# Kernel optimization log

Hardware: AMD Instinct MI355X
Metric: run time of the kernel (lower is better)

## Reference

```python
import jax, jax.numpy as jnp
import numpy as np
from jax import lax

B, N, M, K = 8, 8192, 2000, 16       # batch, raw pts, subsampled pts, neighbors
C1, C2, OUT = 128, 256, 100          # backbone widths, output_embed_size


def _fps(coords, m):
    """Farthest point sampling. coords [B,N,3] -> indices [B,m] (int32)."""
    b, n, _ = coords.shape
    init_last = jnp.zeros((b,), jnp.int32)

    def body(carry, _):
        mind, last = carry
        p = jnp.take_along_axis(coords, last[:, None, None], axis=1)  # [b,1,3]
        d = jnp.sum((coords - p) ** 2, axis=-1)                        # [b,n]
        mind = jnp.minimum(mind, d)
        nxt = jnp.argmax(mind, axis=-1).astype(jnp.int32)
        return (mind, nxt), nxt

    init = (jnp.full((b, n), 1e30, coords.dtype), init_last)
    _, rest = lax.scan(body, init, None, length=m - 1)                 # [m-1,b]
    return jnp.concatenate([init_last[None], rest], axis=0).T          # [b,m]


def _gather(src, idx):
    # src [B,N,C], idx [B,...] -> [B,...,C]
    return jax.vmap(lambda s, i: s[i])(src, idx)


def _knn(q, src, k):
    # squared-distance via |q|^2+|s|^2-2q.s to avoid a [B,M,N,3] intermediate
    d2 = (jnp.sum(q * q, -1)[:, :, None]
          + jnp.sum(src * src, -1)[:, None, :]
          - 2.0 * jnp.einsum('bmd,bnd->bmn', q, src))
    return lax.top_k(-d2, k)[1]                                        # [B,M,k]


def setup_inputs() -> dict:
    key = jax.random.key(0)
    ks = jax.random.split(key, 3)
    x = jax.random.uniform(ks[0], (B, N, 3), jnp.float32)
    W1 = jax.random.normal(ks[1], (6, C1), jnp.float32) * 0.1
    b1 = jnp.zeros((C1,), jnp.float32)
    W2 = jax.random.normal(ks[2], (3 + C1, C2), jnp.float32) * 0.1
    b2 = jnp.zeros((C2,), jnp.float32)
    return {"x": x, "W1": W1, "b1": b1, "W2": W2, "b2": b2}


def reference(x, W1, b1, W2, b2):
    coords = x
    cg = lax.stop_gradient(coords)          # indices are non-differentiable
    fps_idx = _fps(cg, M)                   # [B,M]
    sub = _gather(coords, fps_idx)          # [B,M,3]
    sub_g = lax.stop_gradient(sub)

    # --- point-conv layer 1: neighbors among raw points, feats = coords ---
    idx1 = _knn(sub_g, cg, K)               # [B,M,K]
    ngh = _gather(coords, idx1)             # [B,M,K,3]
    rel1 = ngh - sub[:, :, None, :]
    h1 = jax.nn.relu(jnp.einsum('bmkf,fc->bmkc',
                                jnp.concatenate([rel1, ngh], -1), W1) + b1)
    f1 = jnp.max(h1, axis=2)                # [B,M,C1]

    # --- point-conv layer 2: neighbors among subsampled points ---
    idx2 = _knn(sub_g, sub_g, K)            # [B,M,K]
    ngh2 = _gather(sub, idx2)               # [B,M,K,3]
    rel2 = ngh2 - sub[:, :, None, :]
    fg = _gather(f1, idx2)                  # [B,M,K,C1]
    h2 = jax.nn.relu(jnp.einsum('bmkf,fc->bmkc',
                                jnp.concatenate([rel2, fg], -1), W2) + b2)
    f2 = jnp.max(h2, axis=2)                # [B,M,C2]

    # --- fused adaptive max+avg pool: M % OUT == 0 -> uniform windows ---
    feat = jnp.transpose(f2, (0, 2, 1))     # [B,C2,M]
    windows = feat.reshape(B, C2, OUT, M // OUT)
    return jnp.max(windows, axis=-1) + jnp.mean(windows, axis=-1)  # [B,C2,OUT]
```

## Files before the change

### kernel.cpp

```cpp
#include <hip/hip_runtime.h>

#define B_    8
#define N_    8192
#define M_    2000
#define K_    16
#define C1_   128
#define C2_   256
#define OUT_  100
#define SUBP_ 2048

__global__ __launch_bounds__(256) void prep_kernel(const float* __restrict__ x,
                                                   float4* __restrict__ coords4,
                                                   float4* __restrict__ sub4) {
    int i = blockIdx.x * 256 + threadIdx.x;
    if (i < B_ * N_) {
        float xx = x[i*3+0], yy = x[i*3+1], zz = x[i*3+2];
        float ss = fmaf(zz, zz, fmaf(yy, yy, xx*xx));
        coords4[i] = make_float4(xx, yy, zz, ss);
    }
    if (i < B_ * (SUBP_ - M_)) {
        int b = i / (SUBP_ - M_), j = i % (SUBP_ - M_);
        sub4[b*SUBP_ + M_ + j] = make_float4(1e15f, 1e15f, 1e15f, 3e30f);
    }
}

#define FPS_T 512
#define FPS_P 16

__device__ __forceinline__ unsigned long long umax64(unsigned long long a, unsigned long long b) {
    return a > b ? a : b;
}

template<int CTRL>
__device__ __forceinline__ unsigned long long dpp_max_u64(unsigned long long v) {
    int lo = __builtin_amdgcn_update_dpp(0, (int)(unsigned)(v & 0xFFFFFFFFull), CTRL, 0xF, 0xF, true);
    int hi = __builtin_amdgcn_update_dpp(0, (int)(v >> 32),                     CTRL, 0xF, 0xF, true);
    unsigned long long o = ((unsigned long long)(unsigned)hi << 32) | (unsigned)lo;
    return umax64(v, o);
}

__device__ __forceinline__ int spread3(int v) {
    return (v & 1) | ((v & 2) << 2) | ((v & 4) << 4);
}

__global__ __launch_bounds__(FPS_T, 1) void fps_kernel(const float4* __restrict__ coords4,
                                                       float4* __restrict__ sub4) {
    int b = blockIdx.x;
    int t = threadIdx.x;
    int w = t >> 6, lane = t & 63;
    const float4* C = coords4 + b * N_;

    __shared__ float4 Clds[N_];
    __shared__ unsigned short sidx[N_];
    __shared__ unsigned int hist[512];
    __shared__ __align__(16) unsigned long long wkey[2][8];

    if (t < 512) hist[t] = 0u;
    __syncthreads();

    int cellv[FPS_P];
#pragma unroll
    for (int j = 0; j < FPS_P; ++j) {
        int i = t + j*FPS_T;
        float4 p = C[i];
        Clds[i] = p;
        int cx = (int)(p.x * 8.0f); cx = cx < 0 ? 0 : (cx > 7 ? 7 : cx);
        int cy = (int)(p.y * 8.0f); cy = cy < 0 ? 0 : (cy > 7 ? 7 : cy);
        int cz = (int)(p.z * 8.0f); cz = cz < 0 ? 0 : (cz > 7 ? 7 : cz);
        int cell = (spread3(cx) << 2) | (spread3(cy) << 1) | spread3(cz);
        cellv[j] = cell;
        atomicAdd(&hist[cell], 1u);
    }
    __syncthreads();

    if (w == 0) {
        unsigned loc[8], tot = 0u;
#pragma unroll
        for (int c2 = 0; c2 < 8; ++c2) { loc[c2] = hist[lane*8 + c2]; tot += loc[c2]; }
        unsigned pre = tot;
#pragma unroll
        for (int d = 1; d < 64; d <<= 1) {
            unsigned o = __shfl_up(pre, d, 64);
            if (lane >= (unsigned)d) pre += o;
        }
        unsigned run = pre - tot;
#pragma unroll
        for (int c2 = 0; c2 < 8; ++c2) { unsigned v = loc[c2]; hist[lane*8 + c2] = run; run += v; }
    }
    __syncthreads();

#pragma unroll
    for (int j = 0; j < FPS_P; ++j) {
        int i = t + j*FPS_T;
        unsigned pos = atomicAdd(&hist[cellv[j]], 1u);
        sidx[pos] = (unsigned short)i;
    }
    __syncthreads();

    float px_[FPS_P], py_[FPS_P], pz_[FPS_P], mind[FPS_P];
    unsigned inv_[FPS_P];
    float bx0 =  1e30f, by0 =  1e30f, bz0 =  1e30f;
    float bx1 = -1e30f, by1 = -1e30f, bz1 = -1e30f;
#pragma unroll
    for (int j = 0; j < FPS_P; ++j) {
        int o = (int)sidx[t*FPS_P + j];
        float4 p = Clds[o];
        px_[j] = p.x; py_[j] = p.y; pz_[j] = p.z;
        mind[j] = 1e30f;
        inv_[j] = 0xFFFFFFFFu - (unsigned)o;
        bx0 = fminf(bx0, p.x); bx1 = fmaxf(bx1, p.x);
        by0 = fminf(by0, p.y); by1 = fmaxf(by1, p.y);
        bz0 = fminf(bz0, p.z); bz1 = fmaxf(bz1, p.z);
    }

    float4 P0 = Clds[0];
    if (t == 0) sub4[b*SUBP_] = P0;
    float Px = P0.x, Py = P0.y, Pz = P0.z;
    unsigned long long ckey = ((unsigned long long)__float_as_uint(1e30f) << 32);

    for (int i = 1; i < M_; ++i) {
        float qx = fminf(fmaxf(Px, bx0), bx1);
        float qy = fminf(fmaxf(Py, by0), by1);
        float qz = fminf(fmaxf(Pz, bz0), bz1);
        float ddx = Px - qx, ddy = Py - qy, ddz = Pz - qz;
        float dminsq = fmaf(ddz, ddz, fmaf(ddy, ddy, ddx*ddx));
        float maxm = __uint_as_float((unsigned)(ckey >> 32));
        if (dminsq * 0.999999f < maxm) {
            float runmax = -3.4e38f;
#pragma unroll
            for (int j = 0; j < FPS_P; ++j) {
                float dx = px_[j] - Px, dy = py_[j] - Py, dz = pz_[j] - Pz;
                float d = fmaf(dz, dz, fmaf(dy, dy, dx*dx));
                float m = fminf(mind[j], d);
                mind[j] = m;
                runmax = fmaxf(runmax, m);
            }
            unsigned ib = 0u;
#pragma unroll
            for (int j = 0; j < FPS_P; ++j) {
                unsigned cand = inv_[j] > ib ? inv_[j] : ib;
                ib = (mind[j] == runmax) ? cand : ib;
            }
            ckey = ((unsigned long long)__float_as_uint(runmax) << 32) | (unsigned long long)ib;
        }
        unsigned long long best = ckey;
        best = dpp_max_u64<0x111>(best);
        best = dpp_max_u64<0x112>(best);
        best = dpp_max_u64<0x114>(best);
        best = dpp_max_u64<0x118>(best);
        best = dpp_max_u64<0x142>(best);
        best = dpp_max_u64<0x143>(best);
        if (lane == 63) wkey[i & 1][w] = best;
        __syncthreads();
        const ulonglong2* wk2 = (const ulonglong2*)wkey[i & 1];
        ulonglong2 q0 = wk2[0], q1 = wk2[1], q2 = wk2[2], q3 = wk2[3];
        unsigned long long gk = umax64(umax64(umax64(q0.x, q0.y), umax64(q1.x, q1.y)),
                                       umax64(umax64(q2.x, q2.y), umax64(q3.x, q3.y)));
        int last = (int)(0xFFFFFFFFu - (unsigned)(gk & 0xFFFFFFFFull));
        float4 P4 = Clds[last];
        Px = P4.x; Py = P4.y; Pz = P4.z;
        if (t == 0) sub4[b*SUBP_ + i] = P4;
    }
}

template<int NCH, int PITCH>
__global__ __launch_bounds__(256) void knn_kernel(const float4* __restrict__ cand,
                                                  const float4* __restrict__ qarr,
                                                  int* __restrict__ outIdx) {
    int lane = threadIdx.x & 63;
    int q = blockIdx.x * 4 + (threadIdx.x >> 6);
    int b = q / M_, m = q % M_;
    const float4* Cb = cand + b * PITCH;
    float4 Q = qarr[b * SUBP_ + m];

    float v[16];
#pragma unroll
    for (int tt = 0; tt < 16; ++tt) v[tt] = 3.4e38f;

#pragma unroll 2
    for (int j = 0; j < NCH; ++j) {
        float4 c = Cb[j*64 + lane];
        float dot = fmaf(c.z, Q.z, fmaf(c.y, Q.y, c.x * Q.x));
        float d = fmaf(-2.0f, dot, Q.w + c.w);
        v[15] = fminf(v[15], d);
#pragma unroll
        for (int tt = 15; tt >= 1; --tt) {
            float lo = fminf(v[tt-1], v[tt]);
            float hi = fmaxf(v[tt-1], v[tt]);
            v[tt-1] = lo; v[tt] = hi;
        }
    }

    float T = 0.0f;
    for (int r = 0; r < 16; ++r) {
        float g = v[0];
#pragma unroll
        for (int s = 1; s < 64; s <<= 1) g = fminf(g, __shfl_xor(g, s, 64));
        unsigned long long mk = __ballot(v[0] == g);
        int fl = __ffsll(mk) - 1;
        if (lane == fl) {
#pragma unroll
            for (int tt = 0; tt < 15; ++tt) v[tt] = v[tt+1];
            v[15] = 3.4e38f;
        }
        T = g;
    }

    unsigned long long mlt = (1ull << lane) - 1ull;
    int base = q * K_;
    int cnt = 0;
    for (int j = 0; j < NCH; ++j) {
        float4 c = Cb[j*64 + lane];
        float dot = fmaf(c.z, Q.z, fmaf(c.y, Q.y, c.x * Q.x));
        float d = fmaf(-2.0f, dot, Q.w + c.w);
        bool lt = d < T;
        unsigned long long m1 = __ballot(lt);
        if (lt) outIdx[base + cnt + __popcll(m1 & mlt)] = j*64 + lane;
        cnt += __popcll(m1);
    }
    int rem = K_ - cnt;
    for (int j = 0; j < NCH && rem > 0; ++j) {
        float4 c = Cb[j*64 + lane];
        float dot = fmaf(c.z, Q.z, fmaf(c.y, Q.y, c.x * Q.x));
        float d = fmaf(-2.0f, dot, Q.w + c.w);
        bool eq = (d == T);
        unsigned long long m2 = __ballot(eq);
        int bef = __popcll(m2 & mlt);
        if (eq && bef < rem) outIdx[base + cnt + bef] = j*64 + lane;
        int take = __popcll(m2); if (take > rem) take = rem;
        cnt += take; rem -= take;
    }
}

__global__ __launch_bounds__(128) void layer1_kernel(const float4* __restrict__ coords4,
        const float4* __restrict__ sub4, const int* __restrict__ idx1,
        const float* __restrict__ W1, const float* __restrict__ b1,
        float* __restrict__ f1) {
    int q = blockIdx.x;
    int b = q / M_, m = q % M_;
    int c = threadIdx.x;
    __shared__ float4 ngh[K_];
    if (c < K_) ngh[c] = coords4[b*N_ + idx1[q*K_ + c]];
    __syncthreads();
    float4 Q = sub4[b*SUBP_ + m];
    float w0 = W1[c],        w1 = W1[C1_ + c],   w2 = W1[2*C1_ + c];
    float w3 = W1[3*C1_ + c], w4 = W1[4*C1_ + c], w5 = W1[5*C1_ + c];
    float bias = b1[c];
    float mx = -3.4e38f;
#pragma unroll
    for (int k = 0; k < K_; ++k) {
        float4 n = ngh[k];
        float rx = n.x - Q.x, ry = n.y - Q.y, rz = n.z - Q.z;
        float s = rx*w0; s = fmaf(ry,w1,s); s = fmaf(rz,w2,s);
        s = fmaf(n.x,w3,s); s = fmaf(n.y,w4,s); s = fmaf(n.z,w5,s);
        s += bias;
        s = fmaxf(s, 0.0f);
        mx = fmaxf(mx, s);
    }
    f1[q*C1_ + c] = mx;
}

#define FPAD 20
__global__ __launch_bounds__(64) void layer2_kernel(const float4* __restrict__ sub4,
        const float* __restrict__ f1, const int* __restrict__ idx2,
        const float* __restrict__ W2, const float* __restrict__ b2,
        float* __restrict__ f2) {
    int q = blockIdx.x;
    int b = q / M_, m = q % M_;
    int t = threadIdx.x;
    __shared__ __align__(16) float feat[(3 + C1_) * FPAD];
    __shared__ int nidx[K_];
    float4 Q = sub4[b*SUBP_ + m];
    if (t < K_) {
        int ik = idx2[q*K_ + t];
        nidx[t] = ik;
        float4 n = sub4[b*SUBP_ + ik];
        feat[0*FPAD + t] = n.x - Q.x;
        feat[1*FPAD + t] = n.y - Q.y;
        feat[2*FPAD + t] = n.z - Q.z;
    }
    __syncthreads();
    for (int e = t; e < K_ * C1_; e += 64) {
        int k = e >> 7, cc = e & 127;
        feat[(3 + cc)*FPAD + k] = f1[(b*M_ + nidx[k])*C1_ + cc];
    }
    __syncthreads();

    float acc[K_][4];
#pragma unroll
    for (int k = 0; k < K_; ++k) { acc[k][0]=0.f; acc[k][1]=0.f; acc[k][2]=0.f; acc[k][3]=0.f; }
    int c0 = t * 4;
    for (int f = 0; f < 3 + C1_; ++f) {
        float4 w  = *(const float4*)(W2 + f*C2_ + c0);
        const float* row = feat + f*FPAD;
        float4 g0 = *(const float4*)(row + 0);
        float4 g1 = *(const float4*)(row + 4);
        float4 g2 = *(const float4*)(row + 8);
        float4 g3 = *(const float4*)(row + 12);
        float gk[16] = {g0.x,g0.y,g0.z,g0.w, g1.x,g1.y,g1.z,g1.w,
                        g2.x,g2.y,g2.z,g2.w, g3.x,g3.y,g3.z,g3.w};
#pragma unroll
        for (int k = 0; k < K_; ++k) {
            acc[k][0] = fmaf(gk[k], w.x, acc[k][0]);
            acc[k][1] = fmaf(gk[k], w.y, acc[k][1]);
            acc[k][2] = fmaf(gk[k], w.z, acc[k][2]);
            acc[k][3] = fmaf(gk[k], w.w, acc[k][3]);
        }
    }
    float4 bb = *(const float4*)(b2 + c0);
    float mx0 = -3.4e38f, mx1 = -3.4e38f, mx2 = -3.4e38f, mx3 = -3.4e38f;
#pragma unroll
    for (int k = 0; k < K_; ++k) {
        float h0 = fmaxf(acc[k][0] + bb.x, 0.0f);
        float h1 = fmaxf(acc[k][1] + bb.y, 0.0f);
        float h2 = fmaxf(acc[k][2] + bb.z, 0.0f);
        float h3 = fmaxf(acc[k][3] + bb.w, 0.0f);
        mx0 = fmaxf(mx0, h0); mx1 = fmaxf(mx1, h1);
        mx2 = fmaxf(mx2, h2); mx3 = fmaxf(mx3, h3);
    }
    *(float4*)(f2 + q*C2_ + c0) = make_float4(mx0, mx1, mx2, mx3);
}

__global__ __launch_bounds__(256) void pool_kernel(const float* __restrict__ f2,
                                                   float* __restrict__ out) {
    int bo = blockIdx.x;
    int b = bo / OUT_, o = bo % OUT_;
    int c = threadIdx.x;
    float mx = -3.4e38f, sm = 0.0f;
#pragma unroll
    for (int w = 0; w < M_/OUT_; ++w) {
        float v = f2[(b*M_ + o*(M_/OUT_) + w)*C2_ + c];
        mx = fmaxf(mx, v);
        sm += v;
    }
    out[(b*C2_ + c)*OUT_ + o] = mx + sm / (float)(M_/OUT_);
}

extern "C" void kernel_launch(void* const* d_in, const int* in_sizes, int n_in,
                              void* d_out, int out_size, void* d_ws, size_t ws_size,
                              hipStream_t stream) {
    const float* x  = (const float*)d_in[0];
    const float* W1 = (const float*)d_in[1];
    const float* b1 = (const float*)d_in[2];
    const float* W2 = (const float*)d_in[3];
    const float* b2 = (const float*)d_in[4];
    float* out = (float*)d_out;

    char* ws = (char*)d_ws;
    size_t off = 0;
    auto alloc = [&](size_t bytes) {
        void* p = ws + off;
        off += (bytes + 255) & ~(size_t)255;
        return p;
    };
    float4* coords4 = (float4*)alloc((size_t)B_*N_*sizeof(float4));
    float4* sub4    = (float4*)alloc((size_t)B_*SUBP_*sizeof(float4));
    int*    idx1    = (int*)  alloc((size_t)B_*M_*K_*sizeof(int));
    int*    idx2    = (int*)  alloc((size_t)B_*M_*K_*sizeof(int));
    float*  f1      = (float*)alloc((size_t)B_*M_*C1_*sizeof(float));
    float*  f2      = (float*)alloc((size_t)B_*M_*C2_*sizeof(float));

    prep_kernel<<<(B_*N_ + 255)/256, 256, 0, stream>>>(x, coords4, sub4);
    fps_kernel<<<B_, FPS_T, 0, stream>>>(coords4, sub4);
    knn_kernel<N_/64,    N_   ><<<B_*M_/4, 256, 0, stream>>>(coords4, sub4, idx1);
    knn_kernel<SUBP_/64, SUBP_><<<B_*M_/4, 256, 0, stream>>>(sub4,    sub4, idx2);
    layer1_kernel<<<B_*M_, 128, 0, stream>>>(coords4, sub4, idx1, W1, b1, f1);
    layer2_kernel<<<B_*M_,  64, 0, stream>>>(sub4, f1, idx2, W2, b2, f2);
    pool_kernel<<<B_*OUT_, 256, 0, stream>>>(f2, out);
}
```

Measured before the change: 2.228 ms.

## Use per-wave bounding boxes to skip FPS distance updates wave-wide

The FPS kernel now culls at wavefront granularity instead of per thread. Points are assigned to waves by spatial octant, and each wave's bounding box is reduced with shuffles. The cached wave maximum is broadcast with readlane so a whole wave can skip both the distance update and the DPP reduction when the new point cannot affect its minima. This trades finer per-thread culling for uniform, divergence-free skips of the reduction. The tolerance factor was also loosened.

```diff
diff --git a/kernel.cpp b/kernel.cpp
--- a/kernel.cpp
+++ b/kernel.cpp
@@ -97,35 +97,42 @@
     }
     __syncthreads();
 
+    int oct = (w < 4) ? w : 11 - w;
+    int sbase = oct*1024 + lane*FPS_P;
     float px_[FPS_P], py_[FPS_P], pz_[FPS_P], mind[FPS_P];
     unsigned inv_[FPS_P];
-    float bx0 =  1e30f, by0 =  1e30f, bz0 =  1e30f;
-    float bx1 = -1e30f, by1 = -1e30f, bz1 = -1e30f;
+    float wx0 =  1e30f, wy0 =  1e30f, wz0 =  1e30f;
+    float wx1 = -1e30f, wy1 = -1e30f, wz1 = -1e30f;
 #pragma unroll
     for (int j = 0; j < FPS_P; ++j) {
-        int o = (int)sidx[t*FPS_P + j];
+        int o = (int)sidx[sbase + j];
         float4 p = Clds[o];
         px_[j] = p.x; py_[j] = p.y; pz_[j] = p.z;
         mind[j] = 1e30f;
         inv_[j] = 0xFFFFFFFFu - (unsigned)o;
-        bx0 = fminf(bx0, p.x); bx1 = fmaxf(bx1, p.x);
-        by0 = fminf(by0, p.y); by1 = fmaxf(by1, p.y);
-        bz0 = fminf(bz0, p.z); bz1 = fmaxf(bz1, p.z);
+        wx0 = fminf(wx0, p.x); wx1 = fmaxf(wx1, p.x);
+        wy0 = fminf(wy0, p.y); wy1 = fmaxf(wy1, p.y);
+        wz0 = fminf(wz0, p.z); wz1 = fmaxf(wz1, p.z);
+    }
+    for (int s = 1; s < 64; s <<= 1) {
+        wx0 = fminf(wx0, __shfl_xor(wx0, s, 64)); wx1 = fmaxf(wx1, __shfl_xor(wx1, s, 64));
+        wy0 = fminf(wy0, __shfl_xor(wy0, s, 64)); wy1 = fmaxf(wy1, __shfl_xor(wy1, s, 64));
+        wz0 = fminf(wz0, __shfl_xor(wz0, s, 64)); wz1 = fmaxf(wz1, __shfl_xor(wz1, s, 64));
     }
 
     float4 P0 = Clds[0];
     if (t == 0) sub4[b*SUBP_] = P0;
     float Px = P0.x, Py = P0.y, Pz = P0.z;
-    unsigned long long ckey = ((unsigned long long)__float_as_uint(1e30f) << 32);
+    unsigned long long wk = ((unsigned long long)__float_as_uint(1e30f) << 32);
+    float wmaxf = 1e30f;
 
     for (int i = 1; i < M_; ++i) {
-        float qx = fminf(fmaxf(Px, bx0), bx1);
-        float qy = fminf(fmaxf(Py, by0), by1);
-        float qz = fminf(fmaxf(Pz, bz0), bz1);
+        float qx = fminf(fmaxf(Px, wx0), wx1);
+        float qy = fminf(fmaxf(Py, wy0), wy1);
+        float qz = fminf(fmaxf(Pz, wz0), wz1);
         float ddx = Px - qx, ddy = Py - qy, ddz = Pz - qz;
-        float dminsq = fmaf(ddz, ddz, fmaf(ddy, ddy, ddx*ddx));
-        float maxm = __uint_as_float((unsigned)(ckey >> 32));
-        if (dminsq * 0.999999f < maxm) {
+        float dmin2 = fmaf(ddz, ddz, fmaf(ddy, ddy, ddx*ddx));
+        if (dmin2 * 0.99999f < wmaxf) {
             float runmax = -3.4e38f;
 #pragma unroll
             for (int j = 0; j < FPS_P; ++j) {
@@ -141,16 +148,18 @@
                 unsigned cand = inv_[j] > ib ? inv_[j] : ib;
                 ib = (mind[j] == runmax) ? cand : ib;
             }
-            ckey = ((unsigned long long)__float_as_uint(runmax) << 32) | (unsigned long long)ib;
-        }
-        unsigned long long best = ckey;
-        best = dpp_max_u64<0x111>(best);
-        best = dpp_max_u64<0x112>(best);
-        best = dpp_max_u64<0x114>(best);
-        best = dpp_max_u64<0x118>(best);
-        best = dpp_max_u64<0x142>(best);
-        best = dpp_max_u64<0x143>(best);
-        if (lane == 63) wkey[i & 1][w] = best;
+            unsigned long long best = ((unsigned long long)__float_as_uint(runmax) << 32)
+                                    | (unsigned long long)ib;
+            best = dpp_max_u64<0x111>(best);
+            best = dpp_max_u64<0x112>(best);
+            best = dpp_max_u64<0x114>(best);
+            best = dpp_max_u64<0x118>(best);
+            best = dpp_max_u64<0x142>(best);
+            best = dpp_max_u64<0x143>(best);
+            wk = best;
+            wmaxf = __uint_as_float((unsigned)__builtin_amdgcn_readlane((int)(unsigned)(wk >> 32), 63));
+        }
+        if (lane == 63) wkey[i & 1][w] = wk;
         __syncthreads();
         const ulonglong2* wk2 = (const ulonglong2*)wkey[i & 1];
         ulonglong2 q0 = wk2[0], q1 = wk2[1], q2 = wk2[2], q3 = wk2[3];
```

After: 2.152 ms. 3.4% less time.
